# Optimization experiments

Hardware: AMD Instinct MI355X
Metric: run time of the kernel (lower is better)

The kernel has to match this reference:

```python
import jax, jax.numpy as jnp
import numpy as np

B = 131072
COUNT = 8
L1, L2, L3 = 512, 16, 32


def setup_inputs() -> dict:
    key = jax.random.key(0)
    ks = jax.random.split(key, 10)
    return {
        "accum": jax.random.normal(ks[0], (B, 2 * (L1 + COUNT)), dtype=jnp.float32),
        "us": jax.random.uniform(ks[1], (B,), dtype=jnp.float32),
        "l1_w": jax.random.normal(ks[2], (L2 * COUNT, 2 * L1), dtype=jnp.float32) * 0.02,
        "l1_b": jax.random.normal(ks[3], (L2 * COUNT,), dtype=jnp.float32) * 0.02,
        "l2_w": jax.random.normal(ks[4], (L3 * COUNT, L2), dtype=jnp.float32) * 0.05,
        "l2_b": jax.random.normal(ks[5], (L3 * COUNT,), dtype=jnp.float32) * 0.05,
        "out_w": jax.random.normal(ks[6], (COUNT, L3), dtype=jnp.float32) * 0.05,
        "out_b": jax.random.normal(ks[7], (COUNT,), dtype=jnp.float32) * 0.05,
        "psqt_indices": jax.random.randint(ks[8], (B,), 0, COUNT),
        "layer_stack_indices": jax.random.randint(ks[9], (B,), 0, COUNT),
    }


def reference(accum, us, l1_w, l1_b, l2_w, l2_b, out_w, out_b,
              psqt_indices, layer_stack_indices):
    n = accum.shape[0]
    rows = jnp.arange(n)
    lsi = layer_stack_indices.astype(jnp.int32)

    # split accumulator: [w_main(512), w_psqt(8), b_main(512), b_psqt(8)]
    w_main = accum[:, :L1]
    w_psqt = accum[:, L1:L1 + COUNT]
    b_main = accum[:, L1 + COUNT:2 * L1 + COUNT]
    b_psqt = accum[:, 2 * L1 + COUNT:]
    main_accum = jnp.concatenate([w_main, b_main], axis=1)  # [B, 1024]

    # LayerStacks: dense compute over all stacks, then per-sample gather
    l1s = (main_accum @ l1_w.T + l1_b).reshape(n, COUNT, L2)
    l1y = jnp.clip(l1s[rows, lsi], 0.0, 1.0)                # [B, L2]
    l2s = (l1y @ l2_w.T + l2_b).reshape(n, COUNT, L3)
    l2y = jnp.clip(l2s[rows, lsi], 0.0, 1.0)                # [B, L3]
    l3s = (l2y @ out_w.T + out_b)                           # [B, COUNT]
    net_out = l3s[rows, lsi][:, None]                       # [B, 1]

    # psqt combine
    pi = psqt_indices.astype(jnp.int32)[:, None]
    wpsqt = jnp.take_along_axis(w_psqt, pi, axis=1)
    bpsqt = jnp.take_along_axis(b_psqt, pi, axis=1)
    us_ = us.reshape(-1, 1)
    return net_out + (wpsqt - bpsqt) * (us_ - 0.5)
```

## Files before the change

kernel.cpp:

```cpp
#include <hip/hip_runtime.h>
#include <hip/hip_bf16.h>

#define NCOUNT 8
#define B_TOTAL 131072
#define W_WIN 1024
#define BLK 256
#define AT_STRIDE 1048

typedef __attribute__((ext_vector_type(8))) short bf16x8;
typedef __attribute__((ext_vector_type(4))) float f32x4;
typedef __attribute__((ext_vector_type(16))) float f32x16;

__device__ inline short bf_cvt(float x) {
    __hip_bfloat16 h = __float2bfloat16(x);
    return *reinterpret_cast<short*>(&h);
}
__device__ inline bf16x8 cvt8(float4 a, float4 b) {
    bf16x8 r;
    r[0] = bf_cvt(a.x); r[1] = bf_cvt(a.y); r[2] = bf_cvt(a.z); r[3] = bf_cvt(a.w);
    r[4] = bf_cvt(b.x); r[5] = bf_cvt(b.y); r[6] = bf_cvt(b.z); r[7] = bf_cvt(b.w);
    return r;
}

__global__ __launch_bounds__(BLK, 2) void nnue_mfma_kernel(
    const float* __restrict__ accum,
    const float* __restrict__ us,
    const float* __restrict__ l1_w,
    const float* __restrict__ l1_b,
    const float* __restrict__ l2_w,
    const float* __restrict__ l2_b,
    const float* __restrict__ out_w,
    const float* __restrict__ out_b,
    const int*   __restrict__ psqt_indices,
    const int*   __restrict__ lsi,
    float*       __restrict__ out)
{
    __shared__ int list[W_WIN];
    __shared__ int cnt;
    __shared__ __align__(16) short At[16][AT_STRIDE];
    __shared__ __align__(16) float psq[2][16][16];
    __shared__ __align__(16) float l1part[4][64][4];
    __shared__ __align__(16) float l1y[16 * 20];

    const int l    = blockIdx.y;
    const int base = blockIdx.x * W_WIN;
    const int tid  = threadIdx.x;
    const int lane = tid & 63;
    const int wid  = tid >> 6;

    if (tid == 0) cnt = 0;
    __syncthreads();
    for (int i = tid; i < W_WIN; i += BLK)
        if (lsi[base + i] == l) list[atomicAdd(&cnt, 1)] = base + i;
    __syncthreads();
    const int n = cnt;
    if (n == 0) return;

    const int jlow  = lane & 15;
    const int g     = lane >> 4;
    const int col32 = lane & 31;
    const int h     = lane >> 5;

    const float* wrow = l1_w + (((size_t)l * 16 + jlow) << 10);
    bf16x8 wfrag[8];
    #pragma unroll
    for (int i = 0; i < 8; ++i) {
        const int kf = (wid * 8 + i) * 32 + g * 8;
        wfrag[i] = cvt8(*(const float4*)(wrow + kf), *(const float4*)(wrow + kf + 4));
    }
    const float* w2row = l2_w + ((size_t)l * 32 + col32) * 16 + h * 8;
    const bf16x8 w2frag = cvt8(*(const float4*)(w2row), *(const float4*)(w2row + 4));
    float w3v[16], b2v[16];
    #pragma unroll
    for (int r = 0; r < 16; ++r) {
        int j2 = (r & 3) + 8 * (r >> 2) + 4 * h;
        w3v[r] = out_w[l * 32 + j2];
        b2v[r] = l2_b[l * 32 + j2];
    }
    const float l1bias = l1_b[l * 16 + jlow];
    const float outb   = out_b[l];

    const int srow  = tid >> 5;
    const int scol8 = tid & 31;
    const int pr    = tid >> 2;
    const int ppart = tid & 3;
    const int psf   = (ppart < 2) ? (512 + 4 * ppart) : (1032 + 4 * (ppart - 2));

    float4 pfa[8], pfb[8];
    float4 pfq;
    float  us_nxt = 0.f; int pi_nxt = 0;
    float  us_cur;       int pi_cur;

    auto issue_pf = [&](int tb) {
        #pragma unroll
        for (int rr = 0; rr < 2; ++rr) {
            const int mi = tb + rr * 8 + srow;
            const float* src = accum + (size_t)list[mi < n ? mi : n - 1] * 1040;
            #pragma unroll
            for (int p = 0; p < 4; ++p) {
                const int sf = 8 * (scol8 + 32 * p) + (p >= 2 ? 8 : 0);
                pfa[rr * 4 + p] = *(const float4*)(src + sf);
                pfb[rr * 4 + p] = *(const float4*)(src + sf + 4);
            }
        }
        if (tid < 64) {
            const int mi = tb + pr;
            const float* src = accum + (size_t)list[mi < n ? mi : n - 1] * 1040;
            pfq = *(const float4*)(src + psf);
        }
        if (wid == 0 && lane < 16) {
            const int mi = tb + jlow;
            const int s  = list[mi < n ? mi : n - 1];
            us_nxt = us[s];
            pi_nxt = psqt_indices[s];
        }
    };

    issue_pf(0);

    int buf = 0;
    for (int tb = 0; tb < n; tb += 16, buf ^= 1) {
        #pragma unroll
        for (int rr = 0; rr < 2; ++rr) {
            const int row = rr * 8 + srow;
            #pragma unroll
            for (int p = 0; p < 4; ++p)
                *(bf16x8*)&At[row][8 * (scol8 + 32 * p)] = cvt8(pfa[rr * 4 + p], pfb[rr * 4 + p]);
        }
        if (tid < 64) *(float4*)&psq[buf][pr][ppart * 4] = pfq;
        __syncthreads();

        us_cur = us_nxt; pi_cur = pi_nxt;
        issue_pf(tb + 16);

        f32x4 acc = {0.f, 0.f, 0.f, 0.f};
        #pragma unroll
        for (int i = 0; i < 8; ++i) {
            const int kf = (wid * 8 + i) * 32 + g * 8;
            bf16x8 afrag = *(const bf16x8*)&At[jlow][kf];
            acc = __builtin_amdgcn_mfma_f32_16x16x32_bf16(afrag, wfrag[i], acc, 0, 0, 0);
        }
        *(f32x4*)&l1part[wid][lane][0] = acc;
        __syncthreads();

        if (wid == 0) {
            f32x4 t0 = *(const f32x4*)&l1part[0][lane][0];
            f32x4 t1 = *(const f32x4*)&l1part[1][lane][0];
            f32x4 t2 = *(const f32x4*)&l1part[2][lane][0];
            f32x4 t3 = *(const f32x4*)&l1part[3][lane][0];
            #pragma unroll
            for (int r = 0; r < 4; ++r) {
                float v = fminf(fmaxf(t0[r] + t1[r] + t2[r] + t3[r] + l1bias, 0.f), 1.f);
                l1y[(g * 4 + r) * 20 + jlow] = v;
            }
            __builtin_amdgcn_wave_barrier();
            asm volatile("s_waitcnt lgkmcnt(0)" ::: "memory");

            const float* lyr = l1y + (col32 & 15) * 20 + h * 8;
            float4 y0 = *(const float4*)(lyr);
            float4 y1 = *(const float4*)(lyr + 4);
            const bf16x8 b2frag = cvt8(y0, y1);

            f32x16 acc2 = {};
            acc2 = __builtin_amdgcn_mfma_f32_32x32x16_bf16(w2frag, b2frag, acc2, 0, 0, 0);

            float partial = 0.f;
            #pragma unroll
            for (int r = 0; r < 16; ++r) {
                float v = fminf(fmaxf(acc2[r] + b2v[r], 0.f), 1.f);
                partial += v * w3v[r];
            }
            partial += __shfl_xor(partial, 32);

            if (lane < 16 && tb + jlow < n) {
                const int s = list[tb + jlow];
                const float wp = psq[buf][jlow][pi_cur];
                const float bp = psq[buf][jlow][8 + pi_cur];
                out[s] = partial + outb + (wp - bp) * (us_cur - 0.5f);
            }
        }
        __syncthreads();
    }
}

extern "C" void kernel_launch(void* const* d_in, const int* in_sizes, int n_in,
                              void* d_out, int out_size, void* d_ws, size_t ws_size,
                              hipStream_t stream) {
    const float* accum = (const float*)d_in[0];
    const float* us    = (const float*)d_in[1];
    const float* l1_w  = (const float*)d_in[2];
    const float* l1_b  = (const float*)d_in[3];
    const float* l2_w  = (const float*)d_in[4];
    const float* l2_b  = (const float*)d_in[5];
    const float* out_w = (const float*)d_in[6];
    const float* out_b = (const float*)d_in[7];
    const int*   psqt  = (const int*)d_in[8];
    const int*   lsi   = (const int*)d_in[9];
    float* out = (float*)d_out;

    dim3 grid(B_TOTAL / W_WIN, NCOUNT);
    nnue_mfma_kernel<<<grid, BLK, 0, stream>>>(
        accum, us, l1_w, l1_b, l2_w, l2_b, out_w, out_b, psqt, lsi, out);
}
```

Baseline: 111.0 us.

## Double-depth register prefetch of accumulator tiles and move epilogue weights to LDS

The single register prefetch buffer becomes two alternating buffers, so loads for the next two 16-row tiles are in flight while the current tile is converted, multiplied and finished. The per-lane l2 bias and output-weight arrays move from registers into a small shared-memory table, freeing VGPRs to hold the second prefetch set. The aim is more outstanding global loads to hide memory latency in this bandwidth-bound gather. The cost is higher register pressure from doubled prefetch storage, which could reduce occupancy or cause spills, plus extra LDS reads in the epilogue.

New measurement: 112.0 us. No clear change (+0.9%).

```diff
diff --git a/kernel.cpp b/kernel.cpp
--- a/kernel.cpp
+++ b/kernel.cpp
@@ -41,6 +41,7 @@
     __shared__ __align__(16) float psq[2][16][16];
     __shared__ __align__(16) float l1part[4][64][4];
     __shared__ __align__(16) float l1y[16 * 20];
+    __shared__ float epiw[64];
 
     const int l    = blockIdx.y;
     const int base = blockIdx.x * W_WIN;
@@ -52,6 +53,8 @@
     __syncthreads();
     for (int i = tid; i < W_WIN; i += BLK)
         if (lsi[base + i] == l) list[atomicAdd(&cnt, 1)] = base + i;
+    if (tid < 64)
+        epiw[tid] = (tid < 32) ? l2_b[l * 32 + tid] : out_w[l * 32 + (tid - 32)];
     __syncthreads();
     const int n = cnt;
     if (n == 0) return;
@@ -70,13 +73,6 @@
     }
     const float* w2row = l2_w + ((size_t)l * 32 + col32) * 16 + h * 8;
     const bf16x8 w2frag = cvt8(*(const float4*)(w2row), *(const float4*)(w2row + 4));
-    float w3v[16], b2v[16];
-    #pragma unroll
-    for (int r = 0; r < 16; ++r) {
-        int j2 = (r & 3) + 8 * (r >> 2) + 4 * h;
-        w3v[r] = out_w[l * 32 + j2];
-        b2v[r] = l2_b[l * 32 + j2];
-    }
     const float l1bias = l1_b[l * 16 + jlow];
     const float outb   = out_b[l];
 
@@ -86,53 +82,48 @@
     const int ppart = tid & 3;
     const int psf   = (ppart < 2) ? (512 + 4 * ppart) : (1032 + 4 * (ppart - 2));
 
-    float4 pfa[8], pfb[8];
-    float4 pfq;
-    float  us_nxt = 0.f; int pi_nxt = 0;
-    float  us_cur;       int pi_cur;
-
-    auto issue_pf = [&](int tb) {
+    float4 pfa0[8], pfb0[8], pfq0; float usn0 = 0.f; int pin0 = 0;
+    float4 pfa1[8], pfb1[8], pfq1; float usn1 = 0.f; int pin1 = 0;
+
+    auto issue_pf = [&](int tbn, float4 (&pa)[8], float4 (&pb)[8], float4& pq,
+                        float& usn, int& pin) {
         #pragma unroll
         for (int rr = 0; rr < 2; ++rr) {
-            const int mi = tb + rr * 8 + srow;
+            const int mi = tbn + rr * 8 + srow;
             const float* src = accum + (size_t)list[mi < n ? mi : n - 1] * 1040;
             #pragma unroll
             for (int p = 0; p < 4; ++p) {
                 const int sf = 8 * (scol8 + 32 * p) + (p >= 2 ? 8 : 0);
-                pfa[rr * 4 + p] = *(const float4*)(src + sf);
-                pfb[rr * 4 + p] = *(const float4*)(src + sf + 4);
+                pa[rr * 4 + p] = *(const float4*)(src + sf);
+                pb[rr * 4 + p] = *(const float4*)(src + sf + 4);
             }
         }
         if (tid < 64) {
-            const int mi = tb + pr;
+            const int mi = tbn + pr;
             const float* src = accum + (size_t)list[mi < n ? mi : n - 1] * 1040;
-            pfq = *(const float4*)(src + psf);
+            pq = *(const float4*)(src + psf);
         }
         if (wid == 0 && lane < 16) {
-            const int mi = tb + jlow;
+            const int mi = tbn + jlow;
             const int s  = list[mi < n ? mi : n - 1];
-            us_nxt = us[s];
-            pi_nxt = psqt_indices[s];
-        }
-    };
-
-    issue_pf(0);
-
-    int buf = 0;
-    for (int tb = 0; tb < n; tb += 16, buf ^= 1) {
+            usn = us[s];
+            pin = psqt_indices[s];
+        }
+    };
+
+    auto stage = [&](const float4 (&pa)[8], const float4 (&pb)[8], const float4& pq,
+                     int qbuf) {
         #pragma unroll
         for (int rr = 0; rr < 2; ++rr) {
             const int row = rr * 8 + srow;
             #pragma unroll
             for (int p = 0; p < 4; ++p)
-                *(bf16x8*)&At[row][8 * (scol8 + 32 * p)] = cvt8(pfa[rr * 4 + p], pfb[rr * 4 + p]);
-        }
-        if (tid < 64) *(float4*)&psq[buf][pr][ppart * 4] = pfq;
-        __syncthreads();
-
-        us_cur = us_nxt; pi_cur = pi_nxt;
-        issue_pf(tb + 16);
-
+                *(bf16x8*)&At[row][8 * (scol8 + 32 * p)] = cvt8(pa[rr * 4 + p], pb[rr * 4 + p]);
+        }
+        if (tid < 64) *(float4*)&psq[qbuf][pr][ppart * 4] = pq;
+    };
+
+    auto compute = [&]() {
         f32x4 acc = {0.f, 0.f, 0.f, 0.f};
         #pragma unroll
         for (int i = 0; i < 8; ++i) {
@@ -141,45 +132,68 @@
             acc = __builtin_amdgcn_mfma_f32_16x16x32_bf16(afrag, wfrag[i], acc, 0, 0, 0);
         }
         *(f32x4*)&l1part[wid][lane][0] = acc;
+    };
+
+    auto epilogue = [&](int tb_, int qbuf, float us_e, int pi_e) {
+        if (wid != 0) return;
+        f32x4 t0 = *(const f32x4*)&l1part[0][lane][0];
+        f32x4 t1 = *(const f32x4*)&l1part[1][lane][0];
+        f32x4 t2 = *(const f32x4*)&l1part[2][lane][0];
+        f32x4 t3 = *(const f32x4*)&l1part[3][lane][0];
+        #pragma unroll
+        for (int r = 0; r < 4; ++r) {
+            float v = fminf(fmaxf(t0[r] + t1[r] + t2[r] + t3[r] + l1bias, 0.f), 1.f);
+            l1y[(g * 4 + r) * 20 + jlow] = v;
+        }
+        __builtin_amdgcn_wave_barrier();
+        asm volatile("s_waitcnt lgkmcnt(0)" ::: "memory");
+
+        const float* lyr = l1y + (col32 & 15) * 20 + h * 8;
+        float4 y0 = *(const float4*)(lyr);
+        float4 y1 = *(const float4*)(lyr + 4);
+        const bf16x8 b2frag = cvt8(y0, y1);
+
+        f32x16 acc2 = {};
+        acc2 = __builtin_amdgcn_mfma_f32_32x32x16_bf16(w2frag, b2frag, acc2, 0, 0, 0);
+
+        float partial = 0.f;
+        #pragma unroll
+        for (int r = 0; r < 16; ++r) {
+            const int j2 = (r & 3) + 8 * (r >> 2) + 4 * h;
+            float v = fminf(fmaxf(acc2[r] + epiw[j2], 0.f), 1.f);
+            partial += v * epiw[32 + j2];
+        }
+        partial += __shfl_xor(partial, 32);
+
+        if (lane < 16 && tb_ + jlow < n) {
+            const int s = list[tb_ + jlow];
+            const float wp = psq[qbuf][jlow][pi_e];
+            const float bp = psq[qbuf][jlow][8 + pi_e];
+            out[s] = partial + outb + (wp - bp) * (us_e - 0.5f);
+        }
+    };
+
+    issue_pf(0, pfa0, pfb0, pfq0, usn0, pin0);
+    if (n > 16) issue_pf(16, pfa1, pfb1, pfq1, usn1, pin1);
+
+    for (int tb = 0; tb < n; tb += 32) {
+        stage(pfa0, pfb0, pfq0, 0);
         __syncthreads();
-
-        if (wid == 0) {
-            f32x4 t0 = *(const f32x4*)&l1part[0][lane][0];
-            f32x4 t1 = *(const f32x4*)&l1part[1][lane][0];
-            f32x4 t2 = *(const f32x4*)&l1part[2][lane][0];
-            f32x4 t3 = *(const f32x4*)&l1part[3][lane][0];
-            #pragma unroll
-            for (int r = 0; r < 4; ++r) {
-                float v = fminf(fmaxf(t0[r] + t1[r] + t2[r] + t3[r] + l1bias, 0.f), 1.f);
-                l1y[(g * 4 + r) * 20 + jlow] = v;
-            }
-            __builtin_amdgcn_wave_barrier();
-            asm volatile("s_waitcnt lgkmcnt(0)" ::: "memory");
-
-            const float* lyr = l1y + (col32 & 15) * 20 + h * 8;
-            float4 y0 = *(const float4*)(lyr);
-            float4 y1 = *(const float4*)(lyr + 4);
-            const bf16x8 b2frag = cvt8(y0, y1);
-
-            f32x16 acc2 = {};
-            acc2 = __builtin_amdgcn_mfma_f32_32x32x16_bf16(w2frag, b2frag, acc2, 0, 0, 0);
-
-            float partial = 0.f;
-            #pragma unroll
-            for (int r = 0; r < 16; ++r) {
-                float v = fminf(fmaxf(acc2[r] + b2v[r], 0.f), 1.f);
-                partial += v * w3v[r];
-            }
-            partial += __shfl_xor(partial, 32);
-
-            if (lane < 16 && tb + jlow < n) {
-                const int s = list[tb + jlow];
-                const float wp = psq[buf][jlow][pi_cur];
-                const float bp = psq[buf][jlow][8 + pi_cur];
-                out[s] = partial + outb + (wp - bp) * (us_cur - 0.5f);
-            }
-        }
+        float us_e = usn0; int pi_e = pin0;
+        if (tb + 32 < n) issue_pf(tb + 32, pfa0, pfb0, pfq0, usn0, pin0);
+        compute();
         __syncthreads();
+        epilogue(tb, 0, us_e, pi_e);
+
+        if (tb + 16 < n) {
+            stage(pfa1, pfb1, pfq1, 1);
+            __syncthreads();
+            us_e = usn1; pi_e = pin1;
+            if (tb + 48 < n) issue_pf(tb + 48, pfa1, pfb1, pfq1, usn1, pin1);
+            compute();
+            __syncthreads();
+            epilogue(tb + 16, 1, us_e, pi_e);
+        }
     }
 }
 
```

## Process 32-row tiles with XOR-swizzled LDS, split epilogue across two waves

Applied to the files above, without the earlier changes.

Doubles the per-iteration tile from 16 to 32 samples, so each wave issues two MFMAs per k-step and reuses its weight fragment across both. The A tile in LDS drops its padded stride for an XOR swizzle to avoid bank conflicts. The L2/L3 epilogue is split across two waves, one per 16-row half, and the trailing barrier is removed by double-buffering the psqt and l1y staging. Other changes: the sample list is stored as 16-bit offsets, and the epilogue weights move from registers to shared memory. In exchange the kernel uses more LDS (64KB tile) and twice the prefetch registers, which may reduce occupancy below the requested 2 blocks per CU.

Measured after the change: 109.2 us. No clear change (-1.6%).

```diff
diff --git a/kernel.cpp b/kernel.cpp
--- a/kernel.cpp
+++ b/kernel.cpp
@@ -5,7 +5,6 @@
 #define B_TOTAL 131072
 #define W_WIN 1024
 #define BLK 256
-#define AT_STRIDE 1048
 
 typedef __attribute__((ext_vector_type(8))) short bf16x8;
 typedef __attribute__((ext_vector_type(4))) float f32x4;
@@ -20,6 +19,10 @@
     r[0] = bf_cvt(a.x); r[1] = bf_cvt(a.y); r[2] = bf_cvt(a.z); r[3] = bf_cvt(a.w);
     r[4] = bf_cvt(b.x); r[5] = bf_cvt(b.y); r[6] = bf_cvt(b.z); r[7] = bf_cvt(b.w);
     return r;
+}
+
+__device__ inline int atx(int row, int kbf) {
+    return (row * 1024 + kbf) ^ ((row & 7) << 3);
 }
 
 __global__ __launch_bounds__(BLK, 2) void nnue_mfma_kernel(
@@ -35,12 +38,13 @@
     const int*   __restrict__ lsi,
     float*       __restrict__ out)
 {
-    __shared__ int list[W_WIN];
+    __shared__ unsigned short list[W_WIN];
     __shared__ int cnt;
-    __shared__ __align__(16) short At[16][AT_STRIDE];
-    __shared__ __align__(16) float psq[2][16][16];
-    __shared__ __align__(16) float l1part[4][64][4];
-    __shared__ __align__(16) float l1y[16 * 20];
+    __shared__ __align__(16) short At[32 * 1024];
+    __shared__ __align__(16) float psq[2][32][16];
+    __shared__ __align__(16) f32x4 l1part[2][3][64];
+    __shared__ __align__(16) float l1y[2][16 * 20];
+    __shared__ float epiw[64];
 
     const int l    = blockIdx.y;
     const int base = blockIdx.x * W_WIN;
@@ -51,7 +55,9 @@
     if (tid == 0) cnt = 0;
     __syncthreads();
     for (int i = tid; i < W_WIN; i += BLK)
-        if (lsi[base + i] == l) list[atomicAdd(&cnt, 1)] = base + i;
+        if (lsi[base + i] == l) list[atomicAdd(&cnt, 1)] = (unsigned short)i;
+    if (tid < 64)
+        epiw[tid] = (tid < 32) ? l2_b[l * 32 + tid] : out_w[l * 32 + (tid - 32)];
     __syncthreads();
     const int n = cnt;
     if (n == 0) return;
@@ -70,13 +76,6 @@
     }
     const float* w2row = l2_w + ((size_t)l * 32 + col32) * 16 + h * 8;
     const bf16x8 w2frag = cvt8(*(const float4*)(w2row), *(const float4*)(w2row + 4));
-    float w3v[16], b2v[16];
-    #pragma unroll
-    for (int r = 0; r < 16; ++r) {
-        int j2 = (r & 3) + 8 * (r >> 2) + 4 * h;
-        w3v[r] = out_w[l * 32 + j2];
-        b2v[r] = l2_b[l * 32 + j2];
-    }
     const float l1bias = l1_b[l * 16 + jlow];
     const float outb   = out_b[l];
 
@@ -86,16 +85,15 @@
     const int ppart = tid & 3;
     const int psf   = (ppart < 2) ? (512 + 4 * ppart) : (1032 + 4 * (ppart - 2));
 
-    float4 pfa[8], pfb[8];
-    float4 pfq;
-    float  us_nxt = 0.f; int pi_nxt = 0;
-    float  us_cur;       int pi_cur;
-
-    auto issue_pf = [&](int tb) {
+    float4 pfa[16], pfb[16], pfq;
+    float usn = 0.f, usc; int pin = 0, pic;
+
+    auto issue_pf = [&](int tbn) {
         #pragma unroll
-        for (int rr = 0; rr < 2; ++rr) {
-            const int mi = tb + rr * 8 + srow;
-            const float* src = accum + (size_t)list[mi < n ? mi : n - 1] * 1040;
+        for (int rr = 0; rr < 4; ++rr) {
+            const int mi = tbn + 8 * rr + srow;
+            const int s  = base + list[mi < n ? mi : n - 1];
+            const float* src = accum + (size_t)s * 1040;
             #pragma unroll
             for (int p = 0; p < 4; ++p) {
                 const int sf = 8 * (scol8 + 32 * p) + (p >= 2 ? 8 : 0);
@@ -103,60 +101,70 @@
                 pfb[rr * 4 + p] = *(const float4*)(src + sf + 4);
             }
         }
-        if (tid < 64) {
-            const int mi = tb + pr;
-            const float* src = accum + (size_t)list[mi < n ? mi : n - 1] * 1040;
+        if (tid < 128) {
+            const int mi = tbn + pr;
+            const float* src = accum + (size_t)(base + list[mi < n ? mi : n - 1]) * 1040;
             pfq = *(const float4*)(src + psf);
         }
-        if (wid == 0 && lane < 16) {
-            const int mi = tb + jlow;
-            const int s  = list[mi < n ? mi : n - 1];
-            us_nxt = us[s];
-            pi_nxt = psqt_indices[s];
+        if (lane < 16 && wid < 2) {
+            const int mi = tbn + wid * 16 + jlow;
+            const int s  = base + list[mi < n ? mi : n - 1];
+            usn = us[s];
+            pin = psqt_indices[s];
         }
     };
 
+    auto stage = [&](int par) {
+        #pragma unroll
+        for (int rr = 0; rr < 4; ++rr) {
+            const int row = 8 * rr + srow;
+            #pragma unroll
+            for (int p = 0; p < 4; ++p)
+                *(bf16x8*)&At[atx(row, 8 * (scol8 + 32 * p))] =
+                    cvt8(pfa[rr * 4 + p], pfb[rr * 4 + p]);
+        }
+        if (tid < 128) *(float4*)&psq[par][pr][ppart * 4] = pfq;
+    };
+
     issue_pf(0);
 
-    int buf = 0;
-    for (int tb = 0; tb < n; tb += 16, buf ^= 1) {
-        #pragma unroll
-        for (int rr = 0; rr < 2; ++rr) {
-            const int row = rr * 8 + srow;
-            #pragma unroll
-            for (int p = 0; p < 4; ++p)
-                *(bf16x8*)&At[row][8 * (scol8 + 32 * p)] = cvt8(pfa[rr * 4 + p], pfb[rr * 4 + p]);
-        }
-        if (tid < 64) *(float4*)&psq[buf][pr][ppart * 4] = pfq;
+    int par = 0;
+    for (int tb = 0; tb < n; tb += 32, par ^= 1) {
+        stage(par);
         __syncthreads();
-
-        us_cur = us_nxt; pi_cur = pi_nxt;
-        issue_pf(tb + 16);
-
-        f32x4 acc = {0.f, 0.f, 0.f, 0.f};
+        usc = usn; pic = pin;
+        if (tb + 32 < n) issue_pf(tb + 32);
+
+        f32x4 a0 = {0.f, 0.f, 0.f, 0.f};
+        f32x4 a1 = {0.f, 0.f, 0.f, 0.f};
         #pragma unroll
         for (int i = 0; i < 8; ++i) {
             const int kf = (wid * 8 + i) * 32 + g * 8;
-            bf16x8 afrag = *(const bf16x8*)&At[jlow][kf];
-            acc = __builtin_amdgcn_mfma_f32_16x16x32_bf16(afrag, wfrag[i], acc, 0, 0, 0);
-        }
-        *(f32x4*)&l1part[wid][lane][0] = acc;
+            bf16x8 f0 = *(const bf16x8*)&At[atx(jlow,      kf)];
+            bf16x8 f1 = *(const bf16x8*)&At[atx(jlow + 16, kf)];
+            a0 = __builtin_amdgcn_mfma_f32_16x16x32_bf16(f0, wfrag[i], a0, 0, 0, 0);
+            a1 = __builtin_amdgcn_mfma_f32_16x16x32_bf16(f1, wfrag[i], a1, 0, 0, 0);
+        }
+        if (wid != 0) l1part[0][wid - 1][lane] = a0;
+        if (wid != 1) l1part[1][wid == 0 ? 0 : wid - 1][lane] = a1;
         __syncthreads();
 
-        if (wid == 0) {
-            f32x4 t0 = *(const f32x4*)&l1part[0][lane][0];
-            f32x4 t1 = *(const f32x4*)&l1part[1][lane][0];
-            f32x4 t2 = *(const f32x4*)&l1part[2][lane][0];
-            f32x4 t3 = *(const f32x4*)&l1part[3][lane][0];
+        if (wid < 2) {
+            const int grp = wid;
+            const f32x4 own = (wid == 0) ? a0 : a1;
+            const f32x4 t0 = l1part[grp][0][lane];
+            const f32x4 t1 = l1part[grp][1][lane];
+            const f32x4 t2 = l1part[grp][2][lane];
+            float* ly = l1y[grp];
             #pragma unroll
             for (int r = 0; r < 4; ++r) {
-                float v = fminf(fmaxf(t0[r] + t1[r] + t2[r] + t3[r] + l1bias, 0.f), 1.f);
-                l1y[(g * 4 + r) * 20 + jlow] = v;
+                float v = fminf(fmaxf(own[r] + t0[r] + t1[r] + t2[r] + l1bias, 0.f), 1.f);
+                ly[(g * 4 + r) * 20 + jlow] = v;
             }
             __builtin_amdgcn_wave_barrier();
             asm volatile("s_waitcnt lgkmcnt(0)" ::: "memory");
 
-            const float* lyr = l1y + (col32 & 15) * 20 + h * 8;
+            const float* lyr = ly + (col32 & 15) * 20 + h * 8;
             float4 y0 = *(const float4*)(lyr);
             float4 y1 = *(const float4*)(lyr + 4);
             const bf16x8 b2frag = cvt8(y0, y1);
@@ -167,19 +175,20 @@
             float partial = 0.f;
             #pragma unroll
             for (int r = 0; r < 16; ++r) {
-                float v = fminf(fmaxf(acc2[r] + b2v[r], 0.f), 1.f);
-                partial += v * w3v[r];
+                const int j2 = (r & 3) + 8 * (r >> 2) + 4 * h;
+                float v = fminf(fmaxf(acc2[r] + epiw[j2], 0.f), 1.f);
+                partial += v * epiw[32 + j2];
             }
             partial += __shfl_xor(partial, 32);
 
-            if (lane < 16 && tb + jlow < n) {
-                const int s = list[tb + jlow];
-                const float wp = psq[buf][jlow][pi_cur];
-                const float bp = psq[buf][jlow][8 + pi_cur];
-                out[s] = partial + outb + (wp - bp) * (us_cur - 0.5f);
-            }
-        }
-        __syncthreads();
+            const int mi = tb + grp * 16 + jlow;
+            if (lane < 16 && mi < n) {
+                const int s = base + list[mi];
+                const float wp = psq[par][grp * 16 + jlow][pic];
+                const float bp = psq[par][grp * 16 + jlow][8 + pic];
+                out[s] = partial + outb + (wp - bp) * (usc - 0.5f);
+            }
+        }
     }
 }
 
```
